# Optimization experiments

Hardware: AMD Instinct MI355X
Metric: run time of the kernel (lower is better)

Reference implementation:

```python
import jax, jax.numpy as jnp
import numpy as np

D_MODEL = 1024
H = 16
D_HEAD = D_MODEL // H


def setup_inputs() -> dict:
    key = jax.random.key(0)
    ks = jax.random.split(key, 9)
    B, S = 2, 2048
    x = jax.random.normal(ks[0], (B, S, D_MODEL), dtype=jnp.float32)
    s = 1.0 / np.sqrt(D_HEAD)
    # per-head Q/K/V linears, stacked: W[h, out, in], b[h, out] (torch Linear: y = x W^T + b)
    Wq = jax.random.normal(ks[1], (H, D_HEAD, D_HEAD), dtype=jnp.float32) * s
    bq = jax.random.normal(ks[2], (H, D_HEAD), dtype=jnp.float32) * 0.01
    Wk = jax.random.normal(ks[3], (H, D_HEAD, D_HEAD), dtype=jnp.float32) * s
    bk = jax.random.normal(ks[4], (H, D_HEAD), dtype=jnp.float32) * 0.01
    Wv = jax.random.normal(ks[5], (H, D_HEAD, D_HEAD), dtype=jnp.float32) * s
    bv = jax.random.normal(ks[6], (H, D_HEAD), dtype=jnp.float32) * 0.01
    Wo = jax.random.normal(ks[7], (D_MODEL, D_MODEL), dtype=jnp.float32) / np.sqrt(D_MODEL)
    bo = jax.random.normal(ks[8], (D_MODEL,), dtype=jnp.float32) * 0.01
    return {"x": x, "Wq": Wq, "bq": bq, "Wk": Wk, "bk": bk,
            "Wv": Wv, "bv": bv, "Wo": Wo, "bo": bo}


def reference(x, Wq, bq, Wk, bk, Wv, bv, Wo, bo):
    B, S, D = x.shape
    xh = x.reshape(B, S, H, D_HEAD)  # split along feature dim, head-major
    q = jnp.einsum('bshi,hoi->bsho', xh, Wq) + bq
    k = jnp.einsum('bshi,hoi->bsho', xh, Wk) + bk
    v = jnp.einsum('bshi,hoi->bsho', xh, Wv) + bv
    scale = 1.0 / jnp.sqrt(jnp.asarray(D_HEAD, dtype=x.dtype))  # source scales by sqrt(d_model//h)
    scores = jnp.einsum('bqhd,bkhd->bhqk', q, k) * scale
    causal = jnp.tril(jnp.ones((S, S), dtype=bool))
    scores = jnp.where(causal, scores, -jnp.inf)
    attn = jax.nn.softmax(scores, axis=-1)
    out = jnp.einsum('bhqk,bkhd->bqhd', attn, v).reshape(B, S, D)
    return out @ Wo.T + bo
```

## Files before the change

kernel.cpp:

```cpp
#include <hip/hip_runtime.h>
#include <cstddef>

#define Bc 2
#define Sc 2048
#define Dc 1024
#define Hc 16
#define QSC 0.18033688011112042f

typedef short short8 __attribute__((ext_vector_type(8)));
typedef float floatx4 __attribute__((ext_vector_type(4)));
typedef unsigned short ushort_t;

#if __has_builtin(__builtin_amdgcn_exp2f)
#define EXP2F(x) __builtin_amdgcn_exp2f(x)
#else
#define EXP2F(x) exp2f(x)
#endif

__device__ __forceinline__ unsigned pack2bf(float a, float b) {
    unsigned ua = __float_as_uint(a) + 0x8000u;
    unsigned ub = __float_as_uint(b) + 0x8000u;
    return __builtin_amdgcn_perm(ub, ua, 0x07060302u);
}
__device__ __forceinline__ ushort_t f2bf(float f) {
    return (ushort_t)((__float_as_uint(f) + 0x8000u) >> 16);
}

__global__ __launch_bounds__(256) void qkv_kernel(
    const float* __restrict__ x,
    const float* __restrict__ Wq, const float* __restrict__ Wk, const float* __restrict__ Wv,
    const float* __restrict__ bq, const float* __restrict__ bk, const float* __restrict__ bv,
    ushort_t* __restrict__ Qb, ushort_t* __restrict__ Kf, ushort_t* __restrict__ Vf)
{
    const int blk = blockIdx.x;
    const int st = blk & 31, h = (blk >> 5) & 15, b = blk >> 9;
    const int bh = b * Hc + h, s0 = st * 64;
    const int tid = threadIdx.x, wid = tid >> 6, lane = tid & 63;
    const int lr = lane & 15, quad = lane >> 4;

    __shared__ ushort_t Xs[64 * 72];
    __shared__ ushort_t Wsh[3 * 64 * 72];

    {
        int row = tid >> 2, cg = tid & 3;
        const float* xp = x + ((size_t)(b * Sc + s0 + row)) * Dc + h * 64 + cg * 16;
        float4 v0 = *(const float4*)xp;
        float4 v1 = *(const float4*)(xp + 4);
        float4 v2 = *(const float4*)(xp + 8);
        float4 v3 = *(const float4*)(xp + 12);
        uint4 p0, p1;
        p0.x = pack2bf(v0.x, v0.y); p0.y = pack2bf(v0.z, v0.w);
        p0.z = pack2bf(v1.x, v1.y); p0.w = pack2bf(v1.z, v1.w);
        p1.x = pack2bf(v2.x, v2.y); p1.y = pack2bf(v2.z, v2.w);
        p1.z = pack2bf(v3.x, v3.y); p1.w = pack2bf(v3.z, v3.w);
        *(uint4*)(Xs + row * 72 + cg * 16) = p0;
        *(uint4*)(Xs + row * 72 + cg * 16 + 8) = p1;
    }
    {
#pragma unroll
        for (int s = 0; s < 6; ++s) {
            int c = tid + s * 256;
            int w = c >> 9, rem = c & 511, row = rem >> 3, part = rem & 7;
            const float* wp = (w == 0 ? Wq : (w == 1 ? Wk : Wv))
                              + (size_t)h * 4096 + row * 64 + part * 8;
            float4 v0 = *(const float4*)wp;
            float4 v1 = *(const float4*)(wp + 4);
            uint4 o;
            o.x = pack2bf(v0.x, v0.y); o.y = pack2bf(v0.z, v0.w);
            o.z = pack2bf(v1.x, v1.y); o.w = pack2bf(v1.z, v1.w);
            *(uint4*)(Wsh + (w * 64 + row) * 72 + part * 8) = o;
        }
    }
    __syncthreads();

    short8 af0 = *(const short8*)(Xs + (wid * 16 + lr) * 72 + quad * 8);
    short8 af1 = *(const short8*)(Xs + (wid * 16 + lr) * 72 + 32 + quad * 8);

    const float* bias3[3] = {bq + h * 64, bk + h * 64, bv + h * 64};
    const int row = tid >> 2, cg = tid & 3;

#pragma unroll
    for (int w = 0; w < 3; ++w) {
        ushort_t* Ot = Wsh + w * 64 * 72;
        short8 bf0[4], bf1[4];
#pragma unroll
        for (int n = 0; n < 4; ++n) {
            const ushort_t* wrow = Ot + (n * 16 + lr) * 72;
            bf0[n] = *(const short8*)(wrow + quad * 8);
            bf1[n] = *(const short8*)(wrow + 32 + quad * 8);
        }
        floatx4 acc[4];
#pragma unroll
        for (int n = 0; n < 4; ++n) {
            floatx4 z = {0.f, 0.f, 0.f, 0.f};
            acc[n] = __builtin_amdgcn_mfma_f32_16x16x32_bf16(af0, bf0[n], z, 0, 0, 0);
            acc[n] = __builtin_amdgcn_mfma_f32_16x16x32_bf16(af1, bf1[n], acc[n], 0, 0, 0);
        }
        __syncthreads();
        if (w < 2) {
#pragma unroll
            for (int n = 0; n < 4; ++n) {
                float bias = bias3[w][n * 16 + lr];
#pragma unroll
                for (int r = 0; r < 4; ++r) {
                    float val = acc[n][r] + bias;
                    if (w == 0) val *= QSC;
                    Ot[(wid * 16 + quad * 4 + r) * 72 + n * 16 + lr] = f2bf(val);
                }
            }
        } else {
#pragma unroll
            for (int n = 0; n < 4; ++n) {
                float bias = bias3[2][n * 16 + lr];
                uint2 pw;
                pw.x = pack2bf(acc[n][0] + bias, acc[n][1] + bias);
                pw.y = pack2bf(acc[n][2] + bias, acc[n][3] + bias);
                *(uint2*)(Ot + (n * 16 + lr) * 72 + wid * 16 + quad * 4) = pw;
            }
        }
        __syncthreads();
        if (w == 0) {
            const ushort_t* srcp = Ot + row * 72 + cg * 16;
            uint4 d0 = *(const uint4*)srcp;
            uint4 d1 = *(const uint4*)(srcp + 8);
            ushort_t* dst = Qb + ((size_t)bh * Sc + s0 + row) * 64 + cg * 16;
            *(uint4*)dst = d0;
            *(uint4*)(dst + 8) = d1;
        } else if (w == 1) {
            uint4 d0 = *(const uint4*)(Ot + (4 * lr + wid) * 72 + 8 * quad);
            uint4 d1 = *(const uint4*)(Ot + (4 * lr + wid) * 72 + 32 + 8 * quad);
            ushort_t* dstb = Kf + ((size_t)(bh * 32 + st)) * 4096 + wid * 1024 + lane * 8;
            *(uint4*)dstb = d0;
            *(uint4*)(dstb + 512) = d1;
        } else {
            uint4 d0 = *(const uint4*)(Ot + (wid * 16 + lr) * 72 + 16 * quad);
            uint4 d1 = *(const uint4*)(Ot + (wid * 16 + lr) * 72 + 16 * quad + 8);
            ushort_t* dstb = Vf + ((size_t)(bh * 32 + st)) * 4096 + wid * 1024 + lane * 8;
            *(uint4*)dstb = d0;
            *(uint4*)(dstb + 512) = d1;
        }
    }
}

__global__ __launch_bounds__(256, 3) void attn_kernel(
    const ushort_t* __restrict__ Qg, const ushort_t* __restrict__ Kfg,
    const ushort_t* __restrict__ Vfg, ushort_t* __restrict__ Actx)
{
    const int blk = blockIdx.x;
    const int x = blk & 7;
    const int bh = ((blk >> 3) & 3) * 8 + x;
    const int fbase = (blk >> 5) & 7;
    const int f = (blk < 256) ? fbase : 15 - fbase;
    const int b = bh >> 4, h = bh & 15;
    const int qta = 31 - f, qtb = f;
    const int s0a = qta * 64, s0b = qtb * 64;
    const int tid = threadIdx.x, wid = tid >> 6, lane = tid & 63;
    const int lr = lane & 15, quad = lane >> 4;

    const ushort_t* Kfb = Kfg + (size_t)bh * 32 * 4096 + lane * 8;
    const ushort_t* Vfb = Vfg + (size_t)bh * 32 * 4096 + lane * 8;

    const ushort_t* QrA = Qg + ((size_t)bh * Sc + s0a + wid * 16 + lr) * 64;
    const ushort_t* QrB = Qg + ((size_t)bh * Sc + s0b + wid * 16 + lr) * 64;
    short8 qfa0 = *(const short8*)(QrA + quad * 8);
    short8 qfa1 = *(const short8*)(QrA + 32 + quad * 8);
    short8 qfb0 = *(const short8*)(QrB + quad * 8);
    short8 qfb1 = *(const short8*)(QrB + 32 + quad * 8);

    floatx4 oA[4], oB[4];
    float lA = 0.f, lB = 0.f;
#pragma unroll
    for (int n = 0; n < 4; ++n) { oA[n] = floatx4{0,0,0,0}; oB[n] = floatx4{0,0,0,0}; }

    for (int kt = 0; kt <= qta; ++kt) {
        const bool hasB = (kt <= qtb);
        const ushort_t* Kt = Kfb + (size_t)kt * 4096;
        const ushort_t* Vt = Vfb + (size_t)kt * 4096;

        short8 kf[4][2], vf[4][2];
#pragma unroll
        for (int kg = 0; kg < 4; ++kg) {
            kf[kg][0] = *(const short8*)(Kt + kg * 1024);
            kf[kg][1] = *(const short8*)(Kt + kg * 1024 + 512);
        }
#pragma unroll
        for (int n = 0; n < 4; ++n) {
            vf[n][0] = *(const short8*)(Vt + n * 1024);
            vf[n][1] = *(const short8*)(Vt + n * 1024 + 512);
        }

        floatx4 sA[4], sB[4];
        __builtin_amdgcn_s_setprio(1);
#pragma unroll
        for (int kg = 0; kg < 4; ++kg) {
            floatx4 z = {0.f, 0.f, 0.f, 0.f};
            floatx4 t0 = __builtin_amdgcn_mfma_f32_16x16x32_bf16(kf[kg][0], qfa0, z, 0, 0, 0);
            sA[kg] = __builtin_amdgcn_mfma_f32_16x16x32_bf16(kf[kg][1], qfa1, t0, 0, 0, 0);
        }
        if (hasB) {
#pragma unroll
            for (int kg = 0; kg < 4; ++kg) {
                floatx4 z = {0.f, 0.f, 0.f, 0.f};
                floatx4 t0 = __builtin_amdgcn_mfma_f32_16x16x32_bf16(kf[kg][0], qfb0, z, 0, 0, 0);
                sB[kg] = __builtin_amdgcn_mfma_f32_16x16x32_bf16(kf[kg][1], qfb1, t0, 0, 0, 0);
            }
        }
        __builtin_amdgcn_s_setprio(0);

        const int qrow = wid * 16 + lr;
        if (kt == qta) {
#pragma unroll
            for (int kg = 0; kg < 4; ++kg)
#pragma unroll
                for (int r = 0; r < 4; ++r)
                    if (16 * quad + 4 * r + kg > qrow) sA[kg][r] = -1e30f;
        }
        if (hasB && kt == qtb) {
#pragma unroll
            for (int kg = 0; kg < 4; ++kg)
#pragma unroll
                for (int r = 0; r < 4; ++r)
                    if (16 * quad + 4 * r + kg > qrow) sB[kg][r] = -1e30f;
        }

        {
            float e[4][4];
#pragma unroll
            for (int kg = 0; kg < 4; ++kg)
#pragma unroll
                for (int r = 0; r < 4; ++r) e[kg][r] = EXP2F(sA[kg][r]);
#pragma unroll
            for (int kg = 0; kg < 4; ++kg)
                lA += (e[kg][0] + e[kg][1]) + (e[kg][2] + e[kg][3]);
            union { uint4 u; short8 s; } p0, p1;
            p0.u.x = pack2bf(e[0][0], e[1][0]); p0.u.y = pack2bf(e[2][0], e[3][0]);
            p0.u.z = pack2bf(e[0][1], e[1][1]); p0.u.w = pack2bf(e[2][1], e[3][1]);
            p1.u.x = pack2bf(e[0][2], e[1][2]); p1.u.y = pack2bf(e[2][2], e[3][2]);
            p1.u.z = pack2bf(e[0][3], e[1][3]); p1.u.w = pack2bf(e[2][3], e[3][3]);
            __builtin_amdgcn_s_setprio(1);
#pragma unroll
            for (int n = 0; n < 4; ++n) {
                oA[n] = __builtin_amdgcn_mfma_f32_16x16x32_bf16(p0.s, vf[n][0], oA[n], 0, 0, 0);
                oA[n] = __builtin_amdgcn_mfma_f32_16x16x32_bf16(p1.s, vf[n][1], oA[n], 0, 0, 0);
            }
            __builtin_amdgcn_s_setprio(0);
        }
        if (hasB) {
            float e[4][4];
#pragma unroll
            for (int kg = 0; kg < 4; ++kg)
#pragma unroll
                for (int r = 0; r < 4; ++r) e[kg][r] = EXP2F(sB[kg][r]);
#pragma unroll
            for (int kg = 0; kg < 4; ++kg)
                lB += (e[kg][0] + e[kg][1]) + (e[kg][2] + e[kg][3]);
            union { uint4 u; short8 s; } p0, p1;
            p0.u.x = pack2bf(e[0][0], e[1][0]); p0.u.y = pack2bf(e[2][0], e[3][0]);
            p0.u.z = pack2bf(e[0][1], e[1][1]); p0.u.w = pack2bf(e[2][1], e[3][1]);
            p1.u.x = pack2bf(e[0][2], e[1][2]); p1.u.y = pack2bf(e[2][2], e[3][2]);
            p1.u.z = pack2bf(e[0][3], e[1][3]); p1.u.w = pack2bf(e[2][3], e[3][3]);
            __builtin_amdgcn_s_setprio(1);
#pragma unroll
            for (int n = 0; n < 4; ++n) {
                oB[n] = __builtin_amdgcn_mfma_f32_16x16x32_bf16(p0.s, vf[n][0], oB[n], 0, 0, 0);
                oB[n] = __builtin_amdgcn_mfma_f32_16x16x32_bf16(p1.s, vf[n][1], oB[n], 0, 0, 0);
            }
            __builtin_amdgcn_s_setprio(0);
        }
    }

    lA += __shfl_xor(lA, 16, 64); lA += __shfl_xor(lA, 32, 64);
    lB += __shfl_xor(lB, 16, 64); lB += __shfl_xor(lB, 32, 64);
    float invA = 1.f / lA, invB = 1.f / lB;
#pragma unroll
    for (int r = 0; r < 4; ++r) {
        float iA = __shfl(invA, 4 * quad + r, 64);
        float iB = __shfl(invB, 4 * quad + r, 64);
        int rowA = s0a + wid * 16 + quad * 4 + r;
        int rowB = s0b + wid * 16 + quad * 4 + r;
        ushort_t* dA = Actx + ((size_t)(b * Sc + rowA)) * Dc + h * 64 + lr;
        ushort_t* dB = Actx + ((size_t)(b * Sc + rowB)) * Dc + h * 64 + lr;
#pragma unroll
        for (int n = 0; n < 4; ++n) {
            dA[n * 16] = f2bf(oA[n][r] * iA);
            dB[n * 16] = f2bf(oB[n][r] * iB);
        }
    }
}

__global__ __launch_bounds__(256, 2) void proj_kernel(
    const ushort_t* __restrict__ Ab, const float* __restrict__ WoF,
    const float* __restrict__ bo, float* __restrict__ out)
{
    const int bn = blockIdx.x & 15, bm = blockIdx.x >> 4;
    const int tid = threadIdx.x, wid = tid >> 6, lane = tid & 63;
    const int lr = lane & 15, quad = lane >> 4;
    const int wm = wid * 32;

    __shared__ ushort_t As[128 * 72];
    __shared__ ushort_t Bs[64 * 72];

    floatx4 acc[2][4];
#pragma unroll
    for (int i = 0; i < 2; ++i)
#pragma unroll
        for (int n = 0; n < 4; ++n) acc[i][n] = floatx4{0.f, 0.f, 0.f, 0.f};

    const ushort_t* Ag = Ab + (size_t)bm * 128 * 1024;
    const float* Wg = WoF + (size_t)bn * 64 * 1024;

    const int arow = tid >> 1, acol = (tid & 1) * 32;
    const int brow = tid >> 2, bcol = (tid & 3) * 16;

    short8 a0, a1, a2, a3;
    float4 b0, b1, b2, b3;

    {
        const ushort_t* ap = Ag + (size_t)arow * 1024 + acol;
        a0 = *(const short8*)(ap);      a1 = *(const short8*)(ap + 8);
        a2 = *(const short8*)(ap + 16); a3 = *(const short8*)(ap + 24);
        const float* bp = Wg + (size_t)brow * 1024 + bcol;
        b0 = *(const float4*)(bp);      b1 = *(const float4*)(bp + 4);
        b2 = *(const float4*)(bp + 8);  b3 = *(const float4*)(bp + 12);
        ushort_t* aw = As + arow * 72 + acol;
        *(short8*)(aw) = a0;      *(short8*)(aw + 8) = a1;
        *(short8*)(aw + 16) = a2; *(short8*)(aw + 24) = a3;
        uint4 w0, w1;
        w0.x = pack2bf(b0.x, b0.y); w0.y = pack2bf(b0.z, b0.w);
        w0.z = pack2bf(b1.x, b1.y); w0.w = pack2bf(b1.z, b1.w);
        w1.x = pack2bf(b2.x, b2.y); w1.y = pack2bf(b2.z, b2.w);
        w1.z = pack2bf(b3.x, b3.y); w1.w = pack2bf(b3.z, b3.w);
        ushort_t* bw = Bs + brow * 72 + bcol;
        *(uint4*)(bw) = w0;
        *(uint4*)(bw + 8) = w1;
    }
    __syncthreads();

    for (int k0 = 0; k0 < 1024; k0 += 64) {
        short8 fa0[2], fa1[2], fb[2][4];
#pragma unroll
        for (int kh = 0; kh < 2; ++kh) {
            fa0[kh] = *(const short8*)(As + (wm + lr) * 72 + kh * 32 + quad * 8);
            fa1[kh] = *(const short8*)(As + (wm + 16 + lr) * 72 + kh * 32 + quad * 8);
#pragma unroll
            for (int n = 0; n < 4; ++n)
                fb[kh][n] = *(const short8*)(Bs + (n * 16 + lr) * 72 + kh * 32 + quad * 8);
        }

        if (k0 < 960) {
            int k1 = k0 + 64;
            const ushort_t* ap = Ag + (size_t)arow * 1024 + k1 + acol;
            a0 = *(const short8*)(ap);      a1 = *(const short8*)(ap + 8);
            a2 = *(const short8*)(ap + 16); a3 = *(const short8*)(ap + 24);
            const float* bp = Wg + (size_t)brow * 1024 + k1 + bcol;
            b0 = *(const float4*)(bp);      b1 = *(const float4*)(bp + 4);
            b2 = *(const float4*)(bp + 8);  b3 = *(const float4*)(bp + 12);
        }

#pragma unroll
        for (int kh = 0; kh < 2; ++kh)
#pragma unroll
            for (int n = 0; n < 4; ++n) {
                acc[0][n] = __builtin_amdgcn_mfma_f32_16x16x32_bf16(fa0[kh], fb[kh][n], acc[0][n], 0, 0, 0);
                acc[1][n] = __builtin_amdgcn_mfma_f32_16x16x32_bf16(fa1[kh], fb[kh][n], acc[1][n], 0, 0, 0);
            }
        __syncthreads();
        if (k0 < 960) {
            ushort_t* aw = As + arow * 72 + acol;
            *(short8*)(aw) = a0;      *(short8*)(aw + 8) = a1;
            *(short8*)(aw + 16) = a2; *(short8*)(aw + 24) = a3;
            uint4 w0, w1;
            w0.x = pack2bf(b0.x, b0.y); w0.y = pack2bf(b0.z, b0.w);
            w0.z = pack2bf(b1.x, b1.y); w0.w = pack2bf(b1.z, b1.w);
            w1.x = pack2bf(b2.x, b2.y); w1.y = pack2bf(b2.z, b2.w);
            w1.z = pack2bf(b3.x, b3.y); w1.w = pack2bf(b3.z, b3.w);
            ushort_t* bw = Bs + brow * 72 + bcol;
            *(uint4*)(bw) = w0;
            *(uint4*)(bw + 8) = w1;
            __syncthreads();
        }
    }

#pragma unroll
    for (int i = 0; i < 2; ++i) {
        int mrow = bm * 128 + wm + i * 16 + quad * 4;
#pragma unroll
        for (int n = 0; n < 4; ++n) {
            int col = bn * 64 + n * 16 + lr;
            float bias = bo[col];
#pragma unroll
            for (int r = 0; r < 4; ++r)
                out[(size_t)(mrow + r) * 1024 + col] = acc[i][n][r] + bias;
        }
    }
}

extern "C" void kernel_launch(void* const* d_in, const int* in_sizes, int n_in,
                              void* d_out, int out_size, void* d_ws, size_t ws_size,
                              hipStream_t stream)
{
    (void)in_sizes; (void)n_in; (void)out_size; (void)ws_size;
    const float* x  = (const float*)d_in[0];
    const float* Wq = (const float*)d_in[1];
    const float* bq = (const float*)d_in[2];
    const float* Wk = (const float*)d_in[3];
    const float* bk = (const float*)d_in[4];
    const float* Wv = (const float*)d_in[5];
    const float* bv = (const float*)d_in[6];
    const float* Wo = (const float*)d_in[7];
    const float* bo = (const float*)d_in[8];
    float* out = (float*)d_out;

    const size_t N4 = (size_t)Bc * Hc * Sc * 64;
    ushort_t* base  = (ushort_t*)d_ws;
    ushort_t* Qb    = base;
    ushort_t* Kf    = base + N4;
    ushort_t* Vf    = base + 2 * N4;
    ushort_t* Actx  = base + 3 * N4;

    qkv_kernel<<<dim3(Bc * Hc * (Sc / 64)), dim3(256), 0, stream>>>(
        x, Wq, Wk, Wv, bq, bk, bv, Qb, Kf, Vf);
    attn_kernel<<<dim3(512), dim3(256), 0, stream>>>(Qb, Kf, Vf, Actx);
    proj_kernel<<<dim3(32 * 16), dim3(256), 0, stream>>>(Actx, Wo, bo, out);
}
```

Measured before the change: 141.1 us.

## Double-buffer K fragments in attention loop to prefetch next tile

The attention inner loop now keeps two register buffers for K fragments and issues the loads for tile kt+1 right after the QK^T MFMAs of tile kt, so global load latency overlaps with the softmax and PV work. The loop is manually unrolled by two to swap the buffers without copies. Launch bounds drop from 3 to 2 waves per SIMD to make room for the extra registers, which cuts occupancy and the latency hiding that comes from running more waves.

```diff
diff --git a/kernel.cpp b/kernel.cpp
--- a/kernel.cpp
+++ b/kernel.cpp
@@ -142,7 +142,108 @@
     }
 }
 
-__global__ __launch_bounds__(256, 3) void attn_kernel(
+#define LOADK(dst, t) do {                                                    \
+    const ushort_t* Kt_ = Kfb + (size_t)(t) * 4096;                           \
+    dst[0][0] = *(const short8*)(Kt_);                                        \
+    dst[0][1] = *(const short8*)(Kt_ + 512);                                  \
+    dst[1][0] = *(const short8*)(Kt_ + 1024);                                 \
+    dst[1][1] = *(const short8*)(Kt_ + 1536);                                 \
+    dst[2][0] = *(const short8*)(Kt_ + 2048);                                 \
+    dst[2][1] = *(const short8*)(Kt_ + 2560);                                 \
+    dst[3][0] = *(const short8*)(Kt_ + 3072);                                 \
+    dst[3][1] = *(const short8*)(Kt_ + 3584);                                 \
+} while (0)
+
+#define ATTN_STEP(kc, kn, kt) do {                                            \
+    const bool hasB = ((kt) <= qtb);                                          \
+    const ushort_t* Vt = Vfb + (size_t)(kt) * 4096;                           \
+    short8 vf[4][2];                                                          \
+    _Pragma("unroll")                                                         \
+    for (int n = 0; n < 4; ++n) {                                             \
+        vf[n][0] = *(const short8*)(Vt + n * 1024);                           \
+        vf[n][1] = *(const short8*)(Vt + n * 1024 + 512);                     \
+    }                                                                         \
+    floatx4 sA[4], sB[4];                                                     \
+    __builtin_amdgcn_s_setprio(1);                                            \
+    _Pragma("unroll")                                                         \
+    for (int kg = 0; kg < 4; ++kg) {                                          \
+        floatx4 z = {0.f, 0.f, 0.f, 0.f};                                     \
+        floatx4 t0 = __builtin_amdgcn_mfma_f32_16x16x32_bf16(kc[kg][0], qfa0, z, 0, 0, 0); \
+        sA[kg] = __builtin_amdgcn_mfma_f32_16x16x32_bf16(kc[kg][1], qfa1, t0, 0, 0, 0);    \
+    }                                                                         \
+    if (hasB) {                                                               \
+        _Pragma("unroll")                                                     \
+        for (int kg = 0; kg < 4; ++kg) {                                      \
+            floatx4 z = {0.f, 0.f, 0.f, 0.f};                                 \
+            floatx4 t0 = __builtin_amdgcn_mfma_f32_16x16x32_bf16(kc[kg][0], qfb0, z, 0, 0, 0); \
+            sB[kg] = __builtin_amdgcn_mfma_f32_16x16x32_bf16(kc[kg][1], qfb1, t0, 0, 0, 0);    \
+        }                                                                     \
+    }                                                                         \
+    __builtin_amdgcn_s_setprio(0);                                            \
+            \
+    LOADK(kn, (kt) < qta ? (kt) + 1 : qta);                                   \
+    const int qrow = wid * 16 + lr;                                           \
+    if ((kt) == qta) {                                                        \
+        _Pragma("unroll")                                                     \
+        for (int kg = 0; kg < 4; ++kg)                                        \
+            _Pragma("unroll")                                                 \
+            for (int r = 0; r < 4; ++r)                                       \
+                if (16 * quad + 4 * r + kg > qrow) sA[kg][r] = -1e30f;        \
+    }                                                                         \
+    if (hasB && (kt) == qtb) {                                                \
+        _Pragma("unroll")                                                     \
+        for (int kg = 0; kg < 4; ++kg)                                        \
+            _Pragma("unroll")                                                 \
+            for (int r = 0; r < 4; ++r)                                       \
+                if (16 * quad + 4 * r + kg > qrow) sB[kg][r] = -1e30f;        \
+    }                                                                         \
+    {                                                                         \
+        float e[4][4];                                                        \
+        _Pragma("unroll")                                                     \
+        for (int kg = 0; kg < 4; ++kg)                                        \
+            _Pragma("unroll")                                                 \
+            for (int r = 0; r < 4; ++r) e[kg][r] = EXP2F(sA[kg][r]);          \
+        _Pragma("unroll")                                                     \
+        for (int kg = 0; kg < 4; ++kg)                                        \
+            lA += (e[kg][0] + e[kg][1]) + (e[kg][2] + e[kg][3]);              \
+        union { uint4 u; short8 s; } p0, p1;                                  \
+        p0.u.x = pack2bf(e[0][0], e[1][0]); p0.u.y = pack2bf(e[2][0], e[3][0]); \
+        p0.u.z = pack2bf(e[0][1], e[1][1]); p0.u.w = pack2bf(e[2][1], e[3][1]); \
+        p1.u.x = pack2bf(e[0][2], e[1][2]); p1.u.y = pack2bf(e[2][2], e[3][2]); \
+        p1.u.z = pack2bf(e[0][3], e[1][3]); p1.u.w = pack2bf(e[2][3], e[3][3]); \
+        __builtin_amdgcn_s_setprio(1);                                        \
+        _Pragma("unroll")                                                     \
+        for (int n = 0; n < 4; ++n) {                                         \
+            oA[n] = __builtin_amdgcn_mfma_f32_16x16x32_bf16(p0.s, vf[n][0], oA[n], 0, 0, 0); \
+            oA[n] = __builtin_amdgcn_mfma_f32_16x16x32_bf16(p1.s, vf[n][1], oA[n], 0, 0, 0); \
+        }                                                                     \
+        __builtin_amdgcn_s_setprio(0);                                        \
+    }                                                                         \
+    if (hasB) {                                                               \
+        float e[4][4];                                                        \
+        _Pragma("unroll")                                                     \
+        for (int kg = 0; kg < 4; ++kg)                                        \
+            _Pragma("unroll")                                                 \
+            for (int r = 0; r < 4; ++r) e[kg][r] = EXP2F(sB[kg][r]);          \
+        _Pragma("unroll")                                                     \
+        for (int kg = 0; kg < 4; ++kg)                                        \
+            lB += (e[kg][0] + e[kg][1]) + (e[kg][2] + e[kg][3]);              \
+        union { uint4 u; short8 s; } p0, p1;                                  \
+        p0.u.x = pack2bf(e[0][0], e[1][0]); p0.u.y = pack2bf(e[2][0], e[3][0]); \
+        p0.u.z = pack2bf(e[0][1], e[1][1]); p0.u.w = pack2bf(e[2][1], e[3][1]); \
+        p1.u.x = pack2bf(e[0][2], e[1][2]); p1.u.y = pack2bf(e[2][2], e[3][2]); \
+        p1.u.z = pack2bf(e[0][3], e[1][3]); p1.u.w = pack2bf(e[2][3], e[3][3]); \
+        __builtin_amdgcn_s_setprio(1);                                        \
+        _Pragma("unroll")                                                     \
+        for (int n = 0; n < 4; ++n) {                                         \
+            oB[n] = __builtin_amdgcn_mfma_f32_16x16x32_bf16(p0.s, vf[n][0], oB[n], 0, 0, 0); \
+            oB[n] = __builtin_amdgcn_mfma_f32_16x16x32_bf16(p1.s, vf[n][1], oB[n], 0, 0, 0); \
+        }                                                                     \
+        __builtin_amdgcn_s_setprio(0);                                        \
+    }                                                                         \
+} while (0)
+
+__global__ __launch_bounds__(256, 2) void attn_kernel(
     const ushort_t* __restrict__ Qg, const ushort_t* __restrict__ Kfg,
     const ushort_t* __restrict__ Vfg, ushort_t* __restrict__ Actx)
 {
@@ -172,101 +273,15 @@
 #pragma unroll
     for (int n = 0; n < 4; ++n) { oA[n] = floatx4{0,0,0,0}; oB[n] = floatx4{0,0,0,0}; }
 
-    for (int kt = 0; kt <= qta; ++kt) {
-        const bool hasB = (kt <= qtb);
-        const ushort_t* Kt = Kfb + (size_t)kt * 4096;
-        const ushort_t* Vt = Vfb + (size_t)kt * 4096;
-
-        short8 kf[4][2], vf[4][2];
-#pragma unroll
-        for (int kg = 0; kg < 4; ++kg) {
-            kf[kg][0] = *(const short8*)(Kt + kg * 1024);
-            kf[kg][1] = *(const short8*)(Kt + kg * 1024 + 512);
-        }
-#pragma unroll
-        for (int n = 0; n < 4; ++n) {
-            vf[n][0] = *(const short8*)(Vt + n * 1024);
-            vf[n][1] = *(const short8*)(Vt + n * 1024 + 512);
-        }
-
-        floatx4 sA[4], sB[4];
-        __builtin_amdgcn_s_setprio(1);
-#pragma unroll
-        for (int kg = 0; kg < 4; ++kg) {
-            floatx4 z = {0.f, 0.f, 0.f, 0.f};
-            floatx4 t0 = __builtin_amdgcn_mfma_f32_16x16x32_bf16(kf[kg][0], qfa0, z, 0, 0, 0);
-            sA[kg] = __builtin_amdgcn_mfma_f32_16x16x32_bf16(kf[kg][1], qfa1, t0, 0, 0, 0);
-        }
-        if (hasB) {
-#pragma unroll
-            for (int kg = 0; kg < 4; ++kg) {
-                floatx4 z = {0.f, 0.f, 0.f, 0.f};
-                floatx4 t0 = __builtin_amdgcn_mfma_f32_16x16x32_bf16(kf[kg][0], qfb0, z, 0, 0, 0);
-                sB[kg] = __builtin_amdgcn_mfma_f32_16x16x32_bf16(kf[kg][1], qfb1, t0, 0, 0, 0);
-            }
-        }
-        __builtin_amdgcn_s_setprio(0);
-
-        const int qrow = wid * 16 + lr;
-        if (kt == qta) {
-#pragma unroll
-            for (int kg = 0; kg < 4; ++kg)
-#pragma unroll
-                for (int r = 0; r < 4; ++r)
-                    if (16 * quad + 4 * r + kg > qrow) sA[kg][r] = -1e30f;
-        }
-        if (hasB && kt == qtb) {
-#pragma unroll
-            for (int kg = 0; kg < 4; ++kg)
-#pragma unroll
-                for (int r = 0; r < 4; ++r)
-                    if (16 * quad + 4 * r + kg > qrow) sB[kg][r] = -1e30f;
-        }
-
-        {
-            float e[4][4];
-#pragma unroll
-            for (int kg = 0; kg < 4; ++kg)
-#pragma unroll
-                for (int r = 0; r < 4; ++r) e[kg][r] = EXP2F(sA[kg][r]);
-#pragma unroll
-            for (int kg = 0; kg < 4; ++kg)
-                lA += (e[kg][0] + e[kg][1]) + (e[kg][2] + e[kg][3]);
-            union { uint4 u; short8 s; } p0, p1;
-            p0.u.x = pack2bf(e[0][0], e[1][0]); p0.u.y = pack2bf(e[2][0], e[3][0]);
-            p0.u.z = pack2bf(e[0][1], e[1][1]); p0.u.w = pack2bf(e[2][1], e[3][1]);
-            p1.u.x = pack2bf(e[0][2], e[1][2]); p1.u.y = pack2bf(e[2][2], e[3][2]);
-            p1.u.z = pack2bf(e[0][3], e[1][3]); p1.u.w = pack2bf(e[2][3], e[3][3]);
-            __builtin_amdgcn_s_setprio(1);
-#pragma unroll
-            for (int n = 0; n < 4; ++n) {
-                oA[n] = __builtin_amdgcn_mfma_f32_16x16x32_bf16(p0.s, vf[n][0], oA[n], 0, 0, 0);
-                oA[n] = __builtin_amdgcn_mfma_f32_16x16x32_bf16(p1.s, vf[n][1], oA[n], 0, 0, 0);
-            }
-            __builtin_amdgcn_s_setprio(0);
-        }
-        if (hasB) {
-            float e[4][4];
-#pragma unroll
-            for (int kg = 0; kg < 4; ++kg)
-#pragma unroll
-                for (int r = 0; r < 4; ++r) e[kg][r] = EXP2F(sB[kg][r]);
-#pragma unroll
-            for (int kg = 0; kg < 4; ++kg)
-                lB += (e[kg][0] + e[kg][1]) + (e[kg][2] + e[kg][3]);
-            union { uint4 u; short8 s; } p0, p1;
-            p0.u.x = pack2bf(e[0][0], e[1][0]); p0.u.y = pack2bf(e[2][0], e[3][0]);
-            p0.u.z = pack2bf(e[0][1], e[1][1]); p0.u.w = pack2bf(e[2][1], e[3][1]);
-            p1.u.x = pack2bf(e[0][2], e[1][2]); p1.u.y = pack2bf(e[2][2], e[3][2]);
-            p1.u.z = pack2bf(e[0][3], e[1][3]); p1.u.w = pack2bf(e[2][3], e[3][3]);
-            __builtin_amdgcn_s_setprio(1);
-#pragma unroll
-            for (int n = 0; n < 4; ++n) {
-                oB[n] = __builtin_amdgcn_mfma_f32_16x16x32_bf16(p0.s, vf[n][0], oB[n], 0, 0, 0);
-                oB[n] = __builtin_amdgcn_mfma_f32_16x16x32_bf16(p1.s, vf[n][1], oB[n], 0, 0, 0);
-            }
-            __builtin_amdgcn_s_setprio(0);
-        }
+    short8 kbuf0[4][2], kbuf1[4][2];
+    LOADK(kbuf0, 0);
+
+    int kt = 0;
+    for (;;) {
+        ATTN_STEP(kbuf0, kbuf1, kt);
+        if (++kt > qta) break;
+        ATTN_STEP(kbuf1, kbuf0, kt);
+        if (++kt > qta) break;
     }
 
     lA += __shfl_xor(lA, 16, 64); lA += __shfl_xor(lA, 32, 64);
```

Measured after the change: 138.3 us. No clear change (-1.9%).

## Split paired causal query tiles into one tile per block, raise occupancy

Applied to the files above, without the earlier changes.

The attention kernel stops pairing a long and a short causal query tile in each block and instead gives every block a single 64-row query tile, doubling the grid to 1024 blocks. Blocks are ordered longest-first so heavy tiles start early. The launch bound is raised to 4 waves per SIMD, and the manual bf16 packing is replaced with the hardware v_cvt_pk_bf16_f32 instruction. This trades the K/V fragment reuse between the two paired tiles, and the balanced per-block work that pairing gave, for more parallelism, lower register use and cheaper conversion. The hardware convert may also round differently from the previous add-and-truncate packing.

```diff
diff --git a/kernel.cpp b/kernel.cpp
--- a/kernel.cpp
+++ b/kernel.cpp
@@ -24,6 +24,11 @@
 }
 __device__ __forceinline__ ushort_t f2bf(float f) {
     return (ushort_t)((__float_as_uint(f) + 0x8000u) >> 16);
+}
+__device__ __forceinline__ unsigned cvtpk2bf(float a, float b) {
+    unsigned r;
+    asm("v_cvt_pk_bf16_f32 %0, %1, %2" : "=v"(r) : "v"(a), "v"(b));
+    return r;
 }
 
 __global__ __launch_bounds__(256) void qkv_kernel(
@@ -142,18 +147,16 @@
     }
 }
 
-__global__ __launch_bounds__(256, 3) void attn_kernel(
+__global__ __launch_bounds__(256, 4) void attn_kernel(
     const ushort_t* __restrict__ Qg, const ushort_t* __restrict__ Kfg,
     const ushort_t* __restrict__ Vfg, ushort_t* __restrict__ Actx)
 {
     const int blk = blockIdx.x;
     const int x = blk & 7;
     const int bh = ((blk >> 3) & 3) * 8 + x;
-    const int fbase = (blk >> 5) & 7;
-    const int f = (blk < 256) ? fbase : 15 - fbase;
+    const int qta = 31 - (blk >> 5);
     const int b = bh >> 4, h = bh & 15;
-    const int qta = 31 - f, qtb = f;
-    const int s0a = qta * 64, s0b = qtb * 64;
+    const int s0a = qta * 64;
     const int tid = threadIdx.x, wid = tid >> 6, lane = tid & 63;
     const int lr = lane & 15, quad = lane >> 4;
 
@@ -161,19 +164,15 @@
     const ushort_t* Vfb = Vfg + (size_t)bh * 32 * 4096 + lane * 8;
 
     const ushort_t* QrA = Qg + ((size_t)bh * Sc + s0a + wid * 16 + lr) * 64;
-    const ushort_t* QrB = Qg + ((size_t)bh * Sc + s0b + wid * 16 + lr) * 64;
     short8 qfa0 = *(const short8*)(QrA + quad * 8);
     short8 qfa1 = *(const short8*)(QrA + 32 + quad * 8);
-    short8 qfb0 = *(const short8*)(QrB + quad * 8);
-    short8 qfb1 = *(const short8*)(QrB + 32 + quad * 8);
-
-    floatx4 oA[4], oB[4];
-    float lA = 0.f, lB = 0.f;
-#pragma unroll
-    for (int n = 0; n < 4; ++n) { oA[n] = floatx4{0,0,0,0}; oB[n] = floatx4{0,0,0,0}; }
+
+    floatx4 oA[4];
+    float lA = 0.f;
+#pragma unroll
+    for (int n = 0; n < 4; ++n) oA[n] = floatx4{0, 0, 0, 0};
 
     for (int kt = 0; kt <= qta; ++kt) {
-        const bool hasB = (kt <= qtb);
         const ushort_t* Kt = Kfb + (size_t)kt * 4096;
         const ushort_t* Vt = Vfb + (size_t)kt * 4096;
 
@@ -189,7 +188,7 @@
             vf[n][1] = *(const short8*)(Vt + n * 1024 + 512);
         }
 
-        floatx4 sA[4], sB[4];
+        floatx4 sA[4];
         __builtin_amdgcn_s_setprio(1);
 #pragma unroll
         for (int kg = 0; kg < 4; ++kg) {
@@ -197,30 +196,15 @@
             floatx4 t0 = __builtin_amdgcn_mfma_f32_16x16x32_bf16(kf[kg][0], qfa0, z, 0, 0, 0);
             sA[kg] = __builtin_amdgcn_mfma_f32_16x16x32_bf16(kf[kg][1], qfa1, t0, 0, 0, 0);
         }
-        if (hasB) {
-#pragma unroll
-            for (int kg = 0; kg < 4; ++kg) {
-                floatx4 z = {0.f, 0.f, 0.f, 0.f};
-                floatx4 t0 = __builtin_amdgcn_mfma_f32_16x16x32_bf16(kf[kg][0], qfb0, z, 0, 0, 0);
-                sB[kg] = __builtin_amdgcn_mfma_f32_16x16x32_bf16(kf[kg][1], qfb1, t0, 0, 0, 0);
-            }
-        }
         __builtin_amdgcn_s_setprio(0);
 
-        const int qrow = wid * 16 + lr;
         if (kt == qta) {
+            const int qrow = wid * 16 + lr;
 #pragma unroll
             for (int kg = 0; kg < 4; ++kg)
 #pragma unroll
                 for (int r = 0; r < 4; ++r)
                     if (16 * quad + 4 * r + kg > qrow) sA[kg][r] = -1e30f;
-        }
-        if (hasB && kt == qtb) {
-#pragma unroll
-            for (int kg = 0; kg < 4; ++kg)
-#pragma unroll
-                for (int r = 0; r < 4; ++r)
-                    if (16 * quad + 4 * r + kg > qrow) sB[kg][r] = -1e30f;
         }
 
         {
@@ -233,10 +217,10 @@
             for (int kg = 0; kg < 4; ++kg)
                 lA += (e[kg][0] + e[kg][1]) + (e[kg][2] + e[kg][3]);
             union { uint4 u; short8 s; } p0, p1;
-            p0.u.x = pack2bf(e[0][0], e[1][0]); p0.u.y = pack2bf(e[2][0], e[3][0]);
-            p0.u.z = pack2bf(e[0][1], e[1][1]); p0.u.w = pack2bf(e[2][1], e[3][1]);
-            p1.u.x = pack2bf(e[0][2], e[1][2]); p1.u.y = pack2bf(e[2][2], e[3][2]);
-            p1.u.z = pack2bf(e[0][3], e[1][3]); p1.u.w = pack2bf(e[2][3], e[3][3]);
+            p0.u.x = cvtpk2bf(e[0][0], e[1][0]); p0.u.y = cvtpk2bf(e[2][0], e[3][0]);
+            p0.u.z = cvtpk2bf(e[0][1], e[1][1]); p0.u.w = cvtpk2bf(e[2][1], e[3][1]);
+            p1.u.x = cvtpk2bf(e[0][2], e[1][2]); p1.u.y = cvtpk2bf(e[2][2], e[3][2]);
+            p1.u.z = cvtpk2bf(e[0][3], e[1][3]); p1.u.w = cvtpk2bf(e[2][3], e[3][3]);
             __builtin_amdgcn_s_setprio(1);
 #pragma unroll
             for (int n = 0; n < 4; ++n) {
@@ -245,46 +229,19 @@
             }
             __builtin_amdgcn_s_setprio(0);
         }
-        if (hasB) {
-            float e[4][4];
-#pragma unroll
-            for (int kg = 0; kg < 4; ++kg)
-#pragma unroll
-                for (int r = 0; r < 4; ++r) e[kg][r] = EXP2F(sB[kg][r]);
-#pragma unroll
-            for (int kg = 0; kg < 4; ++kg)
-                lB += (e[kg][0] + e[kg][1]) + (e[kg][2] + e[kg][3]);
-            union { uint4 u; short8 s; } p0, p1;
-            p0.u.x = pack2bf(e[0][0], e[1][0]); p0.u.y = pack2bf(e[2][0], e[3][0]);
-            p0.u.z = pack2bf(e[0][1], e[1][1]); p0.u.w = pack2bf(e[2][1], e[3][1]);
-            p1.u.x = pack2bf(e[0][2], e[1][2]); p1.u.y = pack2bf(e[2][2], e[3][2]);
-            p1.u.z = pack2bf(e[0][3], e[1][3]); p1.u.w = pack2bf(e[2][3], e[3][3]);
-            __builtin_amdgcn_s_setprio(1);
-#pragma unroll
-            for (int n = 0; n < 4; ++n) {
-                oB[n] = __builtin_amdgcn_mfma_f32_16x16x32_bf16(p0.s, vf[n][0], oB[n], 0, 0, 0);
-                oB[n] = __builtin_amdgcn_mfma_f32_16x16x32_bf16(p1.s, vf[n][1], oB[n], 0, 0, 0);
-            }
-            __builtin_amdgcn_s_setprio(0);
-        }
-    }
-
-    lA += __shfl_xor(lA, 16, 64); lA += __shfl_xor(lA, 32, 64);
-    lB += __shfl_xor(lB, 16, 64); lB += __shfl_xor(lB, 32, 64);
-    float invA = 1.f / lA, invB = 1.f / lB;
+    }
+
+    lA += __shfl_xor(lA, 16, 64);
+    lA += __shfl_xor(lA, 32, 64);
+    float invA = 1.f / lA;
 #pragma unroll
     for (int r = 0; r < 4; ++r) {
         float iA = __shfl(invA, 4 * quad + r, 64);
-        float iB = __shfl(invB, 4 * quad + r, 64);
         int rowA = s0a + wid * 16 + quad * 4 + r;
-        int rowB = s0b + wid * 16 + quad * 4 + r;
         ushort_t* dA = Actx + ((size_t)(b * Sc + rowA)) * Dc + h * 64 + lr;
-        ushort_t* dB = Actx + ((size_t)(b * Sc + rowB)) * Dc + h * 64 + lr;
-#pragma unroll
-        for (int n = 0; n < 4; ++n) {
+#pragma unroll
+        for (int n = 0; n < 4; ++n)
             dA[n * 16] = f2bf(oA[n][r] * iA);
-            dB[n * 16] = f2bf(oB[n][r] * iB);
-        }
     }
 }
 
@@ -420,6 +377,6 @@
 
     qkv_kernel<<<dim3(Bc * Hc * (Sc / 64)), dim3(256), 0, stream>>>(
         x, Wq, Wk, Wv, bq, bk, bv, Qb, Kf, Vf);
-    attn_kernel<<<dim3(512), dim3(256), 0, stream>>>(Qb, Kf, Vf, Actx);
+    attn_kernel<<<dim3(1024), dim3(256), 0, stream>>>(Qb, Kf, Vf, Actx);
     proj_kernel<<<dim3(32 * 16), dim3(256), 0, stream>>>(Actx, Wo, bo, out);
 }
```

New measurement: 150.1 us. 6.4% more time.
